# Performance work log

Hardware: AMD Instinct MI355X
Metric: run time of the kernel (lower is better)

The kernel has to match this reference:

```python
import jax, jax.numpy as jnp
import numpy as np

NUM_HEADS = 128
QK_NOPE = 128
QK_ROPE = 64
V_HEAD = 128
Q_HEAD_DIM = 192
SOFTMAX_SCALE = 1.0 / np.sqrt(192.0)


def _rope_interleave(x, cos, sin):
    # x: [b,h,s,d]; reorder interleaved pairs to half-split layout then rotate
    b, h, s, d = x.shape
    x = x.reshape(b, h, s, d // 2, 2).swapaxes(3, 4).reshape(b, h, s, d)
    x1, x2 = x[..., : d // 2], x[..., d // 2:]
    rot = jnp.concatenate([-x2, x1], axis=-1)
    return x * cos + rot * sin


def setup_inputs() -> dict:
    key = jax.random.key(0)
    ks = jax.random.split(key, 8)
    bsz, q_len = 16, 1
    q_lora, kv_lora = 1536, 512
    cache_cap = 4096
    start_pos = 2048
    s = 0.05
    q_normed_dn = jax.random.normal(ks[0], (bsz, q_len, q_lora), jnp.float32) * s
    compressed_kv = jax.random.normal(ks[1], (bsz, q_len, kv_lora), jnp.float32) * s
    k_pe = jax.random.normal(ks[2], (bsz, 1, q_len, QK_ROPE), jnp.float32) * s
    position_ids = jnp.full((bsz, q_len), start_pos, dtype=jnp.int64)
    ckv_cache = jax.random.normal(ks[3], (bsz, cache_cap, kv_lora), jnp.float32) * s
    k_pe_cache = jax.random.normal(ks[4], (bsz, cache_cap, QK_ROPE), jnp.float32) * s
    # rope caches over full positions
    pos = jnp.arange(cache_cap, dtype=jnp.float32)
    inv = 1.0 / (10000.0 ** (jnp.arange(0, QK_ROPE, 2, dtype=jnp.float32) / QK_ROPE))
    freqs = pos[:, None] * inv[None, :]
    emb = jnp.concatenate([freqs, freqs], axis=-1)
    sin_cache = jnp.sin(emb)
    cos_cache = jnp.cos(emb)
    wkv_b = jax.random.normal(ks[5], (NUM_HEADS, QK_NOPE + V_HEAD, kv_lora), jnp.float32) * s
    wq_b = jax.random.normal(ks[6], (NUM_HEADS * Q_HEAD_DIM, q_lora), jnp.float32) * s
    return {
        "q_normed_dn": q_normed_dn,
        "compressed_kv": compressed_kv,
        "k_pe": k_pe,
        "position_ids": position_ids,
        "start_pos": start_pos,
        "ckv_cache": ckv_cache,
        "k_pe_cache": k_pe_cache,
        "sin_cache": sin_cache,
        "cos_cache": cos_cache,
        "wkv_b": wkv_b,
        "wq_b": wq_b,
    }


def reference(q_normed_dn, compressed_kv, k_pe, position_ids, start_pos,
              ckv_cache, k_pe_cache, sin_cache, cos_cache, wkv_b, wq_b):
    bsz, q_len, q_lora = q_normed_dn.shape
    kv_lora = compressed_kv.shape[-1]

    # split absorbed query projection
    wq_b_t = wq_b.T.reshape(q_lora, NUM_HEADS, Q_HEAD_DIM)  # [l,h,192]
    q_nope = jnp.einsum('bsl,lhd->bhsd', q_normed_dn, wq_b_t[:, :, :QK_NOPE])
    q_pe = jnp.einsum('bsl,lhd->bhsd', q_normed_dn, wq_b_t[:, :, QK_NOPE:])

    # matrix absorption: q_nope projected into latent space via w_ukv
    w_ukv = wkv_b[:, :QK_NOPE]                         # [h,128,c]
    q_nope = jnp.einsum('bshd,hdc->bshc', q_nope.swapaxes(1, 2), w_ukv)  # [b,s,h,c]

    # RoPE on q_pe and k_pe using gathered cos/sin at position_ids
    cos = cos_cache[position_ids][:, None]   # [b,1,s,d]
    sin = sin_cache[position_ids][:, None]
    q_pe = _rope_interleave(q_pe, cos, sin)            # [b,h,s,64]
    k_pe = _rope_interleave(k_pe, cos, sin)            # [b,1,s,64]
    q_pe = q_pe.swapaxes(1, 2)                         # [b,s,h,64]
    k_pe = k_pe[:, 0]                                  # [b,s,64]

    # append new tokens to caches at start_pos (q_len new tokens)
    ckv_cache = jax.lax.dynamic_update_slice(ckv_cache, compressed_kv, (0, start_pos, 0))
    k_pe_cache = jax.lax.dynamic_update_slice(k_pe_cache, k_pe, (0, start_pos, 0))
    kv_len = start_pos + q_len
    ckv = ckv_cache[:, :kv_len]                        # [b,n,c]
    kpe = k_pe_cache[:, :kv_len]                       # [b,n,64]

    # MLA decode attention in latent space (q_len==1, causal trivially satisfied)
    # scores = q_nope . ckv + q_pe . kpe
    scores = (jnp.einsum('bshc,bnc->bhsn', q_nope, ckv) +
              jnp.einsum('bshd,bnd->bhsn', q_pe, kpe)) * SOFTMAX_SCALE
    probs = jax.nn.softmax(scores, axis=-1)
    o = jnp.einsum('bhsn,bnc->bshc', probs, ckv)       # [b,s,h,c]
    o = o.reshape(bsz * q_len, NUM_HEADS, kv_lora)

    # project latent output to v_head_dim via tail of wkv_b
    attn_output = jnp.einsum('bhc,hdc->bhd', o, wkv_b[:, -V_HEAD:])
    return attn_output
```

## Files before the change

### kernel.cpp

```cpp
#include <hip/hip_runtime.h>
#include <hip/hip_bf16.h>
#include <math.h>

typedef __attribute__((ext_vector_type(8))) short short8x;
typedef __attribute__((ext_vector_type(4))) float f32x4;
typedef __attribute__((ext_vector_type(4))) unsigned short u16x4;
typedef __attribute__((ext_vector_type(8))) unsigned short u16x8;

#define NSPLIT 16
#define NTILE 66
#define KVROWS (NTILE * 32)

__device__ __forceinline__ unsigned short f2bf(float x) {
  unsigned int u = __float_as_uint(x);
  u += 0x7fffu + ((u >> 16) & 1u);
  return (unsigned short)(u >> 16);
}
__device__ __forceinline__ float bf2f(unsigned short u) {
  return __uint_as_float(((unsigned int)u) << 16);
}
__device__ __forceinline__ u16x4 cvt4(float4 v) {
  u16x4 r;
  r[0] = f2bf(v.x); r[1] = f2bf(v.y); r[2] = f2bf(v.z); r[3] = f2bf(v.w);
  return r;
}
__device__ __forceinline__ void gload_lds16(const void* g, void* l) {
  __builtin_amdgcn_global_load_lds(
      (const __attribute__((address_space(1))) unsigned int*)g,
      (__attribute__((address_space(3))) unsigned int*)l, 16, 0, 0);
}

__global__ __launch_bounds__(256, 6) void kA(
    const float* __restrict__ ckvc, const float* __restrict__ kpec,
    const float* __restrict__ ckvn, const float* __restrict__ kpein,
    const float* __restrict__ cosc, const float* __restrict__ sinc,
    const int* __restrict__ sposp, int cap,
    unsigned short* __restrict__ kvbf,
    const float* __restrict__ wq, const float* __restrict__ x,
    float* __restrict__ qpart) {
  const int bx = blockIdx.x;
  const int tid = threadIdx.x;

  if (bx < 1536) {
    const int rowblock = bx >> 2, kq = bx & 3;
    const int lane = tid & 63, wid = tid >> 6;
    const int l15 = lane & 15, lg = lane >> 4;
    const int rowb = rowblock * 64 + wid * 16;
    const float* wrow = wq + (size_t)(rowb + l15) * 1536 + kq * 384 + lg * 8;
    const float* xrow = x + (size_t)l15 * 1536 + kq * 384 + lg * 8;

    f32x4 aHH = (f32x4){0.f, 0.f, 0.f, 0.f};
    f32x4 aHL = (f32x4){0.f, 0.f, 0.f, 0.f};
    f32x4 aLH = (f32x4){0.f, 0.f, 0.f, 0.f};
    f32x4 bHH = (f32x4){0.f, 0.f, 0.f, 0.f};
    f32x4 bHL = (f32x4){0.f, 0.f, 0.f, 0.f};
    f32x4 bLH = (f32x4){0.f, 0.f, 0.f, 0.f};

    float4 wA[2], wB[2], xA[2], xB[2];
#pragma unroll
    for (int i = 0; i < 2; ++i) {
      wA[i] = *(const float4*)(wrow + i * 32);
      wB[i] = *(const float4*)(wrow + i * 32 + 4);
      xA[i] = *(const float4*)(xrow + i * 32);
      xB[i] = *(const float4*)(xrow + i * 32 + 4);
    }

#pragma unroll
    for (int kc = 0; kc < 12; ++kc) {
      const int s = kc & 1;
      const float wf[8] = {wA[s].x, wA[s].y, wA[s].z, wA[s].w,
                           wB[s].x, wB[s].y, wB[s].z, wB[s].w};
      const float xf[8] = {xA[s].x, xA[s].y, xA[s].z, xA[s].w,
                           xB[s].x, xB[s].y, xB[s].z, xB[s].w};
      short8x ah, al, bh, bl;
#pragma unroll
      for (int e = 0; e < 8; ++e) {
        const unsigned int wu = __float_as_uint(wf[e]);
        const float whf = __uint_as_float(wu & 0xffff0000u);
        ah[e] = (short)(wu >> 16);
        al[e] = (short)(__float_as_uint(wf[e] - whf) >> 16);
        const unsigned int xu = __float_as_uint(xf[e]);
        const float xhf = __uint_as_float(xu & 0xffff0000u);
        bh[e] = (short)(xu >> 16);
        bl[e] = (short)(__float_as_uint(xf[e] - xhf) >> 16);
      }
      if (kc + 2 < 12) {
        wA[s] = *(const float4*)(wrow + (kc + 2) * 32);
        wB[s] = *(const float4*)(wrow + (kc + 2) * 32 + 4);
        xA[s] = *(const float4*)(xrow + (kc + 2) * 32);
        xB[s] = *(const float4*)(xrow + (kc + 2) * 32 + 4);
      }
      if (kc & 1) {
        bHH = __builtin_amdgcn_mfma_f32_16x16x32_bf16(ah, bh, bHH, 0, 0, 0);
        bHL = __builtin_amdgcn_mfma_f32_16x16x32_bf16(ah, bl, bHL, 0, 0, 0);
        bLH = __builtin_amdgcn_mfma_f32_16x16x32_bf16(al, bh, bLH, 0, 0, 0);
      } else {
        aHH = __builtin_amdgcn_mfma_f32_16x16x32_bf16(ah, bh, aHH, 0, 0, 0);
        aHL = __builtin_amdgcn_mfma_f32_16x16x32_bf16(ah, bl, aHL, 0, 0, 0);
        aLH = __builtin_amdgcn_mfma_f32_16x16x32_bf16(al, bh, aLH, 0, 0, 0);
      }
    }
    const f32x4 acc = (aHH + bHH) + (aHL + bHL) + (aLH + bLH);
#pragma unroll
    for (int r = 0; r < 4; ++r)
      qpart[(size_t)kq * 393216 + (size_t)l15 * 24576 + rowb + lg * 4 + r] = acc[r];
  } else {
    const int bxx = bx - 1536;
    const int spos = sposp[0];
#pragma unroll
    for (int i = 0; i < 8; ++i) {
      const int u = bxx * 2048 + i * 256 + tid;
      const int b = u / 304128;
      const int r = u - b * 304128;
      const int n = r / 144;
      const int c4 = (r - n * 144) * 4;
      float4 v = make_float4(0.f, 0.f, 0.f, 0.f);
      if (n < spos) {
        if (c4 < 512) v = *(const float4*)(ckvc + ((size_t)b * cap + n) * 512 + c4);
        else          v = *(const float4*)(kpec + ((size_t)b * cap + n) * 64 + (c4 - 512));
      } else if (n == spos) {
        if (c4 < 512) v = *(const float4*)(ckvn + (size_t)b * 512 + c4);
        else {
          const int d = c4 - 512;
          const float* kp = kpein + b * 64;
          float o[4];
          if (d < 32) {
#pragma unroll
            for (int k = 0; k < 4; ++k) {
              int j = d + k;
              o[k] = kp[2 * j] * cosc[spos * 64 + j] - kp[2 * j + 1] * sinc[spos * 64 + j];
            }
          } else {
#pragma unroll
            for (int k = 0; k < 4; ++k) {
              int j = d - 32 + k;
              o[k] = kp[2 * j + 1] * cosc[spos * 64 + j] + kp[2 * j] * sinc[spos * 64 + j];
            }
          }
          v = make_float4(o[0], o[1], o[2], o[3]);
        }
      }
      *(u16x4*)(kvbf + (size_t)u * 4) = cvt4(v);
    }
  }
}

__global__ __launch_bounds__(256) void kB2(
    const float* __restrict__ qpart, const float* __restrict__ wkv,
    const float* __restrict__ cosc, const float* __restrict__ sinc,
    const int* __restrict__ sposp, unsigned short* __restrict__ qcat,
    const unsigned short* __restrict__ kvbf, unsigned short* __restrict__ vT) {
  __shared__ __align__(16) unsigned char shbuf[36864];
  const int bx = blockIdx.x;
  const int tid = threadIdx.x;

  if (bx < 256) {
    float* qs = (float*)shbuf;
    const int h = bx & 127;
    const int half = bx >> 7;
    for (int u = tid; u < 2048; u += 256) {
      int bb = u >> 7, d = u & 127;
      const size_t off = (size_t)bb * 24576 + h * 192 + d;
      qs[u] = qpart[off] + qpart[off + 393216] +
              qpart[off + 786432] + qpart[off + 1179648];
    }
    __syncthreads();
    const int c = half * 256 + tid;
    float acc[16];
#pragma unroll
    for (int bb = 0; bb < 16; ++bb) acc[bb] = 0.f;
    const float* wbase = wkv + (size_t)h * 256 * 512;
    for (int d = 0; d < 128; ++d) {
      const float w = wbase[d * 512 + c];
#pragma unroll
      for (int bb = 0; bb < 16; ++bb) acc[bb] += qs[bb * 128 + d] * w;
    }
#pragma unroll
    for (int bb = 0; bb < 16; ++bb)
      qcat[(size_t)(bb * 128 + h) * 576 + c] = f2bf(acc[bb]);
  } else if (bx < 272) {
    const int b = bx - 256;
    const int pos = sposp[0];
#pragma unroll
    for (int i = 0; i < 16; ++i) {
      int idx = tid + i * 256;
      int h = idx >> 5, j = idx & 31;
      const float cj = cosc[pos * 64 + j];
      const float sj = sinc[pos * 64 + j];
      const size_t base = (size_t)b * 24576 + h * 192 + 128;
      float x0 = qpart[base + 2 * j] + qpart[base + 2 * j + 393216] +
                 qpart[base + 2 * j + 786432] + qpart[base + 2 * j + 1179648];
      float x1 = qpart[base + 2 * j + 1] + qpart[base + 2 * j + 1 + 393216] +
                 qpart[base + 2 * j + 1 + 786432] + qpart[base + 2 * j + 1 + 1179648];
      unsigned short* dst = qcat + (size_t)(b * 128 + h) * 576 + 512;
      dst[j] = f2bf(x0 * cj - x1 * sj);
      dst[j + 32] = f2bf(x1 * cj + x0 * sj);
    }
  } else {
    unsigned short* tile_sh = (unsigned short*)shbuf;
    const int v_ = bx - 272;
    const int b = v_ / NTILE;
    const int tile = v_ - b * NTILE;
    const int wid = tid >> 6;
    const unsigned short* src = kvbf + ((size_t)b * KVROWS + tile * 32) * 576;
#pragma unroll
    for (int i = 0; i < 9; ++i) {
      const int ch = i * 256 + tid;
      const int row = ch / 72, cc = ch - row * 72;
      gload_lds16(src + row * 576 + ((cc ^ (row & 7)) * 8),
                  &tile_sh[(i * 256 + wid * 64) * 8]);
    }
    __syncthreads();
    unsigned short* vdst = vT + ((size_t)b * NTILE + tile) * 18432;
#pragma unroll
    for (int r = 0; r < 9; ++r) {
      const int c = r * 64 + (tid >> 2);
      const int q = tid & 3;
      const int c8 = c >> 3, c7 = c & 7;
      u16x8 w;
#pragma unroll
      for (int j = 0; j < 8; ++j)
        w[j] = tile_sh[(q * 8 + j) * 576 + ((c8 ^ j) << 3) + c7];
      *(u16x8*)(vdst + c * 32 + q * 8) = w;
    }
  }
}

__global__ __launch_bounds__(512, 2) void k4_attn(
    const unsigned short* __restrict__ kvbf, const unsigned short* __restrict__ vT,
    const unsigned short* __restrict__ qcat, const int* __restrict__ sposp,
    unsigned short* __restrict__ opart, float* __restrict__ mlp) {
  __shared__ __align__(16) unsigned short kv_sh[2][32 * 576];
  __shared__ __align__(16) unsigned short vt_sh[2][512 * 32];
  __shared__ __align__(16) unsigned short p_sh[8 * 640];

  const int tid = threadIdx.x;
  const int split = blockIdx.x, b = blockIdx.y;
  const int kvlen = sposp[0] + 1;
  const int lane = tid & 63, wid = tid >> 6;
  const int l15 = lane & 15, lg = lane >> 4;

  const unsigned short* kvb = kvbf + (size_t)b * KVROWS * 576;
  const unsigned short* vtb = vT + (size_t)b * NTILE * 18432;

  const int vro = lane >> 2, vq = lane & 3;
  const int vgq = vq ^ ((vro >> 1) & 3);

  auto STAGE = [&](int pb, int tt) {
    const unsigned short* ksrc = kvb + (size_t)tt * 32 * 576;
    for (int j = wid; j < 36; j += 8) {
      int u = j * 64 + lane;
      int row = u / 72, cc = u - row * 72;
      gload_lds16(ksrc + row * 576 + ((cc ^ (row & 7)) * 8), &kv_sh[pb][j * 512]);
    }
    const unsigned short* vsrc = vtb + (size_t)tt * 18432;
    for (int j = wid; j < 32; j += 8)
      gload_lds16(vsrc + j * 512 + vro * 32 + vgq * 8, &vt_sh[pb][j * 512]);
  };

  STAGE(0, split);

  const int hrow = b * 128 + wid * 16 + l15;
  const unsigned short* qrow = qcat + (size_t)hrow * 576;
  short8x qf[18];
#pragma unroll
  for (int s = 0; s < 18; ++s)
    qf[s] = *(const short8x*)(qrow + s * 32 + lg * 8);

  f32x4 acc[32];
#pragma unroll
  for (int i = 0; i < 32; ++i) acc[i] = (f32x4){0.f, 0.f, 0.f, 0.f};
  float mold[4] = {-1e30f, -1e30f, -1e30f, -1e30f};
  float lsum[4] = {0.f, 0.f, 0.f, 0.f};
  const float C2 = (1.0f / sqrtf(192.0f)) * 1.4426950408889634f;

  const int vrd = ((lg ^ ((l15 >> 1) & 3)) << 3);

  int pb = 0;
  for (int tt = split; tt * 32 < kvlen; tt += NSPLIT, pb ^= 1) {
    __syncthreads();
    if ((tt + NSPLIT) * 32 < kvlen) STAGE(pb ^ 1, tt + NSPLIT);
    const int n0 = tt * 32;

    f32x4 D0 = (f32x4){0.f, 0.f, 0.f, 0.f};
    f32x4 D1 = (f32x4){0.f, 0.f, 0.f, 0.f};
#pragma unroll
    for (int s = 0; s < 18; ++s) {
      const int c8 = (s * 4 + lg) ^ (l15 & 7);
      short8x fb0 = *(const short8x*)&kv_sh[pb][l15 * 576 + c8 * 8];
      short8x fb1 = *(const short8x*)&kv_sh[pb][(16 + l15) * 576 + c8 * 8];
      D0 = __builtin_amdgcn_mfma_f32_16x16x32_bf16(qf[s], fb0, D0, 0, 0, 0);
      D1 = __builtin_amdgcn_mfma_f32_16x16x32_bf16(qf[s], fb1, D1, 0, 0, 0);
    }

    const bool v0 = (n0 + l15) < kvlen;
    const bool v1 = (n0 + 16 + l15) < kvlen;
    float alpha[4];
#pragma unroll
    for (int r = 0; r < 4; ++r) {
      const float t0 = v0 ? D0[r] * C2 : -1e30f;
      const float t1 = v1 ? D1[r] * C2 : -1e30f;
      float mx = fmaxf(t0, t1);
      mx = fmaxf(mx, __shfl_xor(mx, 1, 64));
      mx = fmaxf(mx, __shfl_xor(mx, 2, 64));
      mx = fmaxf(mx, __shfl_xor(mx, 4, 64));
      mx = fmaxf(mx, __shfl_xor(mx, 8, 64));
      const float mn = fmaxf(mold[r], mx);
      alpha[r] = exp2f(mold[r] - mn);
      const float p0 = v0 ? exp2f(t0 - mn) : 0.f;
      const float p1 = v1 ? exp2f(t1 - mn) : 0.f;
      float rs = p0 + p1;
      rs += __shfl_xor(rs, 1, 64);
      rs += __shfl_xor(rs, 2, 64);
      rs += __shfl_xor(rs, 4, 64);
      rs += __shfl_xor(rs, 8, 64);
      lsum[r] = lsum[r] * alpha[r] + rs;
      mold[r] = mn;
      p_sh[wid * 640 + (lg * 4 + r) * 40 + l15] = f2bf(p0);
      p_sh[wid * 640 + (lg * 4 + r) * 40 + 16 + l15] = f2bf(p1);
    }
    const f32x4 av = {alpha[0], alpha[1], alpha[2], alpha[3]};
#pragma unroll
    for (int cg = 0; cg < 32; ++cg) acc[cg] *= av;

    const short8x pa = *(const short8x*)&p_sh[wid * 640 + l15 * 40 + lg * 8];
#pragma unroll
    for (int cg = 0; cg < 32; ++cg) {
      short8x bv = *(const short8x*)&vt_sh[pb][cg * 512 + l15 * 32 + vrd];
      acc[cg] = __builtin_amdgcn_mfma_f32_16x16x32_bf16(pa, bv, acc[cg], 0, 0, 0);
    }
  }

  const int hbm_ = b * 128 + wid * 16 + lg * 4;
  if (l15 == 0) {
#pragma unroll
    for (int r = 0; r < 4; ++r) {
      mlp[(size_t)(hbm_ + r) * (2 * NSPLIT) + split * 2] = mold[r];
      mlp[(size_t)(hbm_ + r) * (2 * NSPLIT) + split * 2 + 1] = lsum[r];
    }
  }

  __syncthreads();
  unsigned short* ep = &kv_sh[0][0] + wid * 8192;
#pragma unroll
  for (int cg = 0; cg < 32; ++cg)
#pragma unroll
    for (int r = 0; r < 4; ++r)
      ep[(lg * 4 + r) * 512 + cg * 16 + l15] = f2bf(acc[cg][r]);
#pragma unroll
  for (int r16 = 0; r16 < 16; ++r16) {
    const int bh = b * 128 + wid * 16 + r16;
    const size_t ob = ((size_t)bh * NSPLIT + split) * 512;
#pragma unroll
    for (int i = 0; i < 2; ++i)
      *(u16x4*)&opart[ob + i * 256 + lane * 4] =
          *(const u16x4*)&ep[r16 * 512 + i * 256 + lane * 4];
  }
}

__global__ __launch_bounds__(512) void kC_out(
    const unsigned short* __restrict__ opart, const float* __restrict__ mlp,
    const float* __restrict__ wkv, float* __restrict__ out) {
  __shared__ float os[16 * 512];
  __shared__ float wsc[16 * 16];
  __shared__ float lsc[16];
  const int h = blockIdx.x;
  const int tid = threadIdx.x;

  if (tid < 16) {
    const int b = tid;
    const float* m = mlp + (size_t)(b * 128 + h) * (2 * NSPLIT);
    float mi[NSPLIT], li[NSPLIT], M = -1e30f;
#pragma unroll
    for (int i = 0; i < NSPLIT; ++i) {
      mi[i] = m[i * 2];
      li[i] = m[i * 2 + 1];
      M = fmaxf(M, mi[i]);
    }
    float Ls = 0.f;
#pragma unroll
    for (int i = 0; i < NSPLIT; ++i) {
      const float w = exp2f(mi[i] - M);
      Ls += li[i] * w;
      wsc[b * NSPLIT + i] = w;
    }
    lsc[b] = Ls;
  }
  __syncthreads();

  for (int u = tid; u < 8192; u += 512) {
    const int b = u >> 9, c = u & 511;
    const unsigned short* op = opart + (size_t)(b * 128 + h) * NSPLIT * 512 + c;
    float o = 0.f;
#pragma unroll
    for (int i = 0; i < NSPLIT; ++i) o += wsc[b * NSPLIT + i] * bf2f(op[i * 512]);
    os[u] = o / lsc[b];
  }
  __syncthreads();

  const int d = tid >> 2, cq = tid & 3;
  const float* wrow = wkv + ((size_t)(h * 256 + 128 + d)) * 512;
  float acc[16];
#pragma unroll
  for (int bb = 0; bb < 16; ++bb) acc[bb] = 0.f;
  for (int i = 0; i < 32; ++i) {
    const int c = cq * 4 + i * 16;
    const float4 w4 = *(const float4*)&wrow[c];
#pragma unroll
    for (int bb = 0; bb < 16; ++bb) {
      const float4 o4 = *(const float4*)&os[bb * 512 + c];
      acc[bb] += w4.x * o4.x + w4.y * o4.y + w4.z * o4.z + w4.w * o4.w;
    }
  }
#pragma unroll
  for (int bb = 0; bb < 16; ++bb) {
    float v = acc[bb];
    v += __shfl_xor(v, 1, 64);
    v += __shfl_xor(v, 2, 64);
    if (cq == 0) out[(size_t)(bb * 128 + h) * 128 + d] = v;
  }
}

extern "C" void kernel_launch(void* const* d_in, const int* in_sizes, int n_in,
                              void* d_out, int out_size, void* d_ws, size_t ws_size,
                              hipStream_t stream) {
  const float* x = (const float*)d_in[0];
  const float* ckvn = (const float*)d_in[1];
  const float* kpein = (const float*)d_in[2];
  const int* sposp = (const int*)d_in[4];
  const float* ckvc = (const float*)d_in[5];
  const float* kpec = (const float*)d_in[6];
  const float* sinc = (const float*)d_in[7];
  const float* cosc = (const float*)d_in[8];
  const float* wkv = (const float*)d_in[9];
  const float* wq = (const float*)d_in[10];
  float* out = (float*)d_out;

  const int cap = in_sizes[5] / (16 * 512);

  float* ws = (float*)d_ws;
  float* qpart = ws;
  float* mlp = ws + 1572864;
  unsigned short* qcat = (unsigned short*)(ws + 1638400);
  unsigned short* kvbf = (unsigned short*)(ws + 2228224);
  unsigned short* vT   = (unsigned short*)(ws + 11960320);
  unsigned short* opart = (unsigned short*)(ws + 21692416);

  kA<<<dim3(1536 + 2376), 256, 0, stream>>>(ckvc, kpec, ckvn, kpein, cosc, sinc,
                                            sposp, cap, kvbf, wq, x, qpart);
  kB2<<<dim3(272 + NTILE * 16), 256, 0, stream>>>(qpart, wkv, cosc, sinc, sposp,
                                                  qcat, kvbf, vT);
  k4_attn<<<dim3(NSPLIT, 16), 512, 0, stream>>>(kvbf, vT, qcat, sposp, opart, mlp);
  kC_out<<<dim3(128), 512, 0, stream>>>(opart, mlp, wkv, out);
}
```

Baseline: 171.0 us.

## Fuse KV transpose into attention kernel, dropping separate vT buffer pass

Removes the kB2 blocks that transposed each bf16 KV tile into a global vT buffer. The attention kernel now builds the transposed V tile in LDS from the already-staged KV tile, with an extra barrier before the PV MMA. This saves a global write and re-read of the transposed cache but adds in-loop LDS transpose work and a sync per tile. Launch bounds drop to one block per CU because of the larger LDS footprint.

```diff
diff --git a/kernel.cpp b/kernel.cpp
--- a/kernel.cpp
+++ b/kernel.cpp
@@ -148,14 +148,12 @@
 __global__ __launch_bounds__(256) void kB2(
     const float* __restrict__ qpart, const float* __restrict__ wkv,
     const float* __restrict__ cosc, const float* __restrict__ sinc,
-    const int* __restrict__ sposp, unsigned short* __restrict__ qcat,
-    const unsigned short* __restrict__ kvbf, unsigned short* __restrict__ vT) {
-  __shared__ __align__(16) unsigned char shbuf[36864];
+    const int* __restrict__ sposp, unsigned short* __restrict__ qcat) {
+  __shared__ float qs[16 * 128];
   const int bx = blockIdx.x;
   const int tid = threadIdx.x;
 
   if (bx < 256) {
-    float* qs = (float*)shbuf;
     const int h = bx & 127;
     const int half = bx >> 7;
     for (int u = tid; u < 2048; u += 256) {
@@ -178,7 +176,7 @@
 #pragma unroll
     for (int bb = 0; bb < 16; ++bb)
       qcat[(size_t)(bb * 128 + h) * 576 + c] = f2bf(acc[bb]);
-  } else if (bx < 272) {
+  } else {
     const int b = bx - 256;
     const int pos = sposp[0];
 #pragma unroll
@@ -196,43 +194,18 @@
       dst[j] = f2bf(x0 * cj - x1 * sj);
       dst[j + 32] = f2bf(x1 * cj + x0 * sj);
     }
-  } else {
-    unsigned short* tile_sh = (unsigned short*)shbuf;
-    const int v_ = bx - 272;
-    const int b = v_ / NTILE;
-    const int tile = v_ - b * NTILE;
-    const int wid = tid >> 6;
-    const unsigned short* src = kvbf + ((size_t)b * KVROWS + tile * 32) * 576;
-#pragma unroll
-    for (int i = 0; i < 9; ++i) {
-      const int ch = i * 256 + tid;
-      const int row = ch / 72, cc = ch - row * 72;
-      gload_lds16(src + row * 576 + ((cc ^ (row & 7)) * 8),
-                  &tile_sh[(i * 256 + wid * 64) * 8]);
-    }
-    __syncthreads();
-    unsigned short* vdst = vT + ((size_t)b * NTILE + tile) * 18432;
-#pragma unroll
-    for (int r = 0; r < 9; ++r) {
-      const int c = r * 64 + (tid >> 2);
-      const int q = tid & 3;
-      const int c8 = c >> 3, c7 = c & 7;
-      u16x8 w;
-#pragma unroll
-      for (int j = 0; j < 8; ++j)
-        w[j] = tile_sh[(q * 8 + j) * 576 + ((c8 ^ j) << 3) + c7];
-      *(u16x8*)(vdst + c * 32 + q * 8) = w;
-    }
-  }
-}
-
-__global__ __launch_bounds__(512, 2) void k4_attn(
-    const unsigned short* __restrict__ kvbf, const unsigned short* __restrict__ vT,
+  }
+}
+
+__global__ __launch_bounds__(512, 1) void k4_attn(
+    const unsigned short* __restrict__ kvbf,
     const unsigned short* __restrict__ qcat, const int* __restrict__ sposp,
     unsigned short* __restrict__ opart, float* __restrict__ mlp) {
-  __shared__ __align__(16) unsigned short kv_sh[2][32 * 576];
-  __shared__ __align__(16) unsigned short vt_sh[2][512 * 32];
-  __shared__ __align__(16) unsigned short p_sh[8 * 640];
+  __shared__ __align__(16) unsigned short lds_all[65536];
+  unsigned short* const kv0 = lds_all;
+  unsigned short* const kv1 = lds_all + 18432;
+  unsigned short* const vt_sh = lds_all + 36864;
+  unsigned short* const p_sh = lds_all + 53248;
 
   const int tid = threadIdx.x;
   const int split = blockIdx.x, b = blockIdx.y;
@@ -241,24 +214,17 @@
   const int l15 = lane & 15, lg = lane >> 4;
 
   const unsigned short* kvb = kvbf + (size_t)b * KVROWS * 576;
-  const unsigned short* vtb = vT + (size_t)b * NTILE * 18432;
-
-  const int vro = lane >> 2, vq = lane & 3;
-  const int vgq = vq ^ ((vro >> 1) & 3);
-
-  auto STAGE = [&](int pb, int tt) {
+
+  auto STAGE = [&](unsigned short* dst, int tt) {
     const unsigned short* ksrc = kvb + (size_t)tt * 32 * 576;
     for (int j = wid; j < 36; j += 8) {
       int u = j * 64 + lane;
       int row = u / 72, cc = u - row * 72;
-      gload_lds16(ksrc + row * 576 + ((cc ^ (row & 7)) * 8), &kv_sh[pb][j * 512]);
-    }
-    const unsigned short* vsrc = vtb + (size_t)tt * 18432;
-    for (int j = wid; j < 32; j += 8)
-      gload_lds16(vsrc + j * 512 + vro * 32 + vgq * 8, &vt_sh[pb][j * 512]);
+      gload_lds16(ksrc + row * 576 + ((cc ^ (row & 7)) * 8), dst + j * 512);
+    }
   };
 
-  STAGE(0, split);
+  STAGE(kv0, split);
 
   const int hrow = b * 128 + wid * 16 + l15;
   const unsigned short* qrow = qcat + (size_t)hrow * 576;
@@ -278,17 +244,32 @@
 
   int pb = 0;
   for (int tt = split; tt * 32 < kvlen; tt += NSPLIT, pb ^= 1) {
+    unsigned short* const kvcur = pb ? kv1 : kv0;
+    unsigned short* const kvnxt = pb ? kv0 : kv1;
     __syncthreads();
-    if ((tt + NSPLIT) * 32 < kvlen) STAGE(pb ^ 1, tt + NSPLIT);
+    if ((tt + NSPLIT) * 32 < kvlen) STAGE(kvnxt, tt + NSPLIT);
     const int n0 = tt * 32;
+
+#pragma unroll
+    for (int r5 = 0; r5 < 5; ++r5) {
+      const int idx = r5 * 512 + tid;
+      if (idx < 2304) {
+        const int c = idx >> 2, q = idx & 3;
+        u16x8 w;
+#pragma unroll
+        for (int j = 0; j < 8; ++j)
+          w[j] = kvcur[(q * 8 + j) * 576 + (((c >> 3) ^ j) << 3) + (c & 7)];
+        *(u16x8*)&vt_sh[c * 32 + ((q ^ ((c >> 1) & 3)) << 3)] = w;
+      }
+    }
 
     f32x4 D0 = (f32x4){0.f, 0.f, 0.f, 0.f};
     f32x4 D1 = (f32x4){0.f, 0.f, 0.f, 0.f};
 #pragma unroll
     for (int s = 0; s < 18; ++s) {
       const int c8 = (s * 4 + lg) ^ (l15 & 7);
-      short8x fb0 = *(const short8x*)&kv_sh[pb][l15 * 576 + c8 * 8];
-      short8x fb1 = *(const short8x*)&kv_sh[pb][(16 + l15) * 576 + c8 * 8];
+      short8x fb0 = *(const short8x*)&kvcur[l15 * 576 + c8 * 8];
+      short8x fb1 = *(const short8x*)&kvcur[(16 + l15) * 576 + c8 * 8];
       D0 = __builtin_amdgcn_mfma_f32_16x16x32_bf16(qf[s], fb0, D0, 0, 0, 0);
       D1 = __builtin_amdgcn_mfma_f32_16x16x32_bf16(qf[s], fb1, D1, 0, 0, 0);
     }
@@ -323,10 +304,12 @@
 #pragma unroll
     for (int cg = 0; cg < 32; ++cg) acc[cg] *= av;
 
+    __syncthreads();
+
     const short8x pa = *(const short8x*)&p_sh[wid * 640 + l15 * 40 + lg * 8];
 #pragma unroll
     for (int cg = 0; cg < 32; ++cg) {
-      short8x bv = *(const short8x*)&vt_sh[pb][cg * 512 + l15 * 32 + vrd];
+      short8x bv = *(const short8x*)&vt_sh[cg * 512 + l15 * 32 + vrd];
       acc[cg] = __builtin_amdgcn_mfma_f32_16x16x32_bf16(pa, bv, acc[cg], 0, 0, 0);
     }
   }
@@ -341,7 +324,7 @@
   }
 
   __syncthreads();
-  unsigned short* ep = &kv_sh[0][0] + wid * 8192;
+  unsigned short* ep = lds_all + wid * 8192;
 #pragma unroll
   for (int cg = 0; cg < 32; ++cg)
 #pragma unroll
@@ -443,13 +426,11 @@
   float* mlp = ws + 1572864;
   unsigned short* qcat = (unsigned short*)(ws + 1638400);
   unsigned short* kvbf = (unsigned short*)(ws + 2228224);
-  unsigned short* vT   = (unsigned short*)(ws + 11960320);
-  unsigned short* opart = (unsigned short*)(ws + 21692416);
+  unsigned short* opart = (unsigned short*)(ws + 11960320);
 
   kA<<<dim3(1536 + 2376), 256, 0, stream>>>(ckvc, kpec, ckvn, kpein, cosc, sinc,
                                             sposp, cap, kvbf, wq, x, qpart);
-  kB2<<<dim3(272 + NTILE * 16), 256, 0, stream>>>(qpart, wkv, cosc, sinc, sposp,
-                                                  qcat, kvbf, vT);
-  k4_attn<<<dim3(NSPLIT, 16), 512, 0, stream>>>(kvbf, vT, qcat, sposp, opart, mlp);
+  kB2<<<dim3(272), 256, 0, stream>>>(qpart, wkv, cosc, sinc, sposp, qcat);
+  k4_attn<<<dim3(NSPLIT, 16), 512, 0, stream>>>(kvbf, qcat, sposp, opart, mlp);
   kC_out<<<dim3(128), 512, 0, stream>>>(opart, mlp, wkv, out);
 }
```

New measurement: 176.6 us. +3.3%, slower.

## Drop KV double buffering in attention kernel to shrink LDS footprint

Applied to the files above, without the earlier changes.

Replaces the double-buffered K and V LDS staging with a single buffer that is loaded synchronously each iteration, bracketed by barriers. The output epilogue is split into two passes so it fits in the smaller shared allocation. This cuts LDS per block roughly in half so two 512-thread blocks could co-reside on a CU. In exchange, global-to-LDS loads no longer overlap with the MFMA work of the previous tile. With only 256 blocks in the grid, the extra occupancy may go unused.

```diff
diff --git a/kernel.cpp b/kernel.cpp
--- a/kernel.cpp
+++ b/kernel.cpp
@@ -230,9 +230,10 @@
     const unsigned short* __restrict__ kvbf, const unsigned short* __restrict__ vT,
     const unsigned short* __restrict__ qcat, const int* __restrict__ sposp,
     unsigned short* __restrict__ opart, float* __restrict__ mlp) {
-  __shared__ __align__(16) unsigned short kv_sh[2][32 * 576];
-  __shared__ __align__(16) unsigned short vt_sh[2][512 * 32];
-  __shared__ __align__(16) unsigned short p_sh[8 * 640];
+  __shared__ __align__(16) unsigned short lds_all[39936];
+  unsigned short* const kv_sh = lds_all;
+  unsigned short* const vt_sh = lds_all + 18432;
+  unsigned short* const p_sh = lds_all + 34816;
 
   const int tid = threadIdx.x;
   const int split = blockIdx.x, b = blockIdx.y;
@@ -246,19 +247,17 @@
   const int vro = lane >> 2, vq = lane & 3;
   const int vgq = vq ^ ((vro >> 1) & 3);
 
-  auto STAGE = [&](int pb, int tt) {
+  auto STAGE = [&](int tt) {
     const unsigned short* ksrc = kvb + (size_t)tt * 32 * 576;
     for (int j = wid; j < 36; j += 8) {
       int u = j * 64 + lane;
       int row = u / 72, cc = u - row * 72;
-      gload_lds16(ksrc + row * 576 + ((cc ^ (row & 7)) * 8), &kv_sh[pb][j * 512]);
+      gload_lds16(ksrc + row * 576 + ((cc ^ (row & 7)) * 8), kv_sh + j * 512);
     }
     const unsigned short* vsrc = vtb + (size_t)tt * 18432;
     for (int j = wid; j < 32; j += 8)
-      gload_lds16(vsrc + j * 512 + vro * 32 + vgq * 8, &vt_sh[pb][j * 512]);
+      gload_lds16(vsrc + j * 512 + vro * 32 + vgq * 8, vt_sh + j * 512);
   };
-
-  STAGE(0, split);
 
   const int hrow = b * 128 + wid * 16 + l15;
   const unsigned short* qrow = qcat + (size_t)hrow * 576;
@@ -276,10 +275,10 @@
 
   const int vrd = ((lg ^ ((l15 >> 1) & 3)) << 3);
 
-  int pb = 0;
-  for (int tt = split; tt * 32 < kvlen; tt += NSPLIT, pb ^= 1) {
-    __syncthreads();
-    if ((tt + NSPLIT) * 32 < kvlen) STAGE(pb ^ 1, tt + NSPLIT);
+  for (int tt = split; tt * 32 < kvlen; tt += NSPLIT) {
+    __syncthreads();
+    STAGE(tt);
+    __syncthreads();
     const int n0 = tt * 32;
 
     f32x4 D0 = (f32x4){0.f, 0.f, 0.f, 0.f};
@@ -287,8 +286,8 @@
 #pragma unroll
     for (int s = 0; s < 18; ++s) {
       const int c8 = (s * 4 + lg) ^ (l15 & 7);
-      short8x fb0 = *(const short8x*)&kv_sh[pb][l15 * 576 + c8 * 8];
-      short8x fb1 = *(const short8x*)&kv_sh[pb][(16 + l15) * 576 + c8 * 8];
+      short8x fb0 = *(const short8x*)&kv_sh[l15 * 576 + c8 * 8];
+      short8x fb1 = *(const short8x*)&kv_sh[(16 + l15) * 576 + c8 * 8];
       D0 = __builtin_amdgcn_mfma_f32_16x16x32_bf16(qf[s], fb0, D0, 0, 0, 0);
       D1 = __builtin_amdgcn_mfma_f32_16x16x32_bf16(qf[s], fb1, D1, 0, 0, 0);
     }
@@ -326,7 +325,7 @@
     const short8x pa = *(const short8x*)&p_sh[wid * 640 + l15 * 40 + lg * 8];
 #pragma unroll
     for (int cg = 0; cg < 32; ++cg) {
-      short8x bv = *(const short8x*)&vt_sh[pb][cg * 512 + l15 * 32 + vrd];
+      short8x bv = *(const short8x*)&vt_sh[cg * 512 + l15 * 32 + vrd];
       acc[cg] = __builtin_amdgcn_mfma_f32_16x16x32_bf16(pa, bv, acc[cg], 0, 0, 0);
     }
   }
@@ -340,21 +339,27 @@
     }
   }
 
-  __syncthreads();
-  unsigned short* ep = &kv_sh[0][0] + wid * 8192;
-#pragma unroll
-  for (int cg = 0; cg < 32; ++cg)
-#pragma unroll
-    for (int r = 0; r < 4; ++r)
-      ep[(lg * 4 + r) * 512 + cg * 16 + l15] = f2bf(acc[cg][r]);
-#pragma unroll
-  for (int r16 = 0; r16 < 16; ++r16) {
-    const int bh = b * 128 + wid * 16 + r16;
-    const size_t ob = ((size_t)bh * NSPLIT + split) * 512;
-#pragma unroll
-    for (int i = 0; i < 2; ++i)
-      *(u16x4*)&opart[ob + i * 256 + lane * 4] =
-          *(const u16x4*)&ep[r16 * 512 + i * 256 + lane * 4];
+#pragma unroll
+  for (int p2 = 0; p2 < 2; ++p2) {
+    __syncthreads();
+    unsigned short* ep = lds_all + wid * 4096;
+    if ((lg >> 1) == p2) {
+#pragma unroll
+      for (int cg = 0; cg < 32; ++cg)
+#pragma unroll
+        for (int r = 0; r < 4; ++r)
+          ep[(((lg & 1) * 4) + r) * 512 + cg * 16 + l15] = f2bf(acc[cg][r]);
+    }
+    __syncthreads();
+#pragma unroll
+    for (int r8 = 0; r8 < 8; ++r8) {
+      const int bh = b * 128 + wid * 16 + p2 * 8 + r8;
+      const size_t ob = ((size_t)bh * NSPLIT + split) * 512;
+#pragma unroll
+      for (int i = 0; i < 2; ++i)
+        *(u16x4*)&opart[ob + i * 256 + lane * 4] =
+            *(const u16x4*)&ep[r8 * 512 + i * 256 + lane * 4];
+    }
   }
 }
 
```

New measurement: 173.0 us. Within noise of the previous version (+1.2%).

## Fuse KV bf16 conversion and V transpose into kA via LDS tile staging

Applied to the files above, without the earlier changes.

The KV-cache conversion in kA now works per 32-row tile. Each tile is staged in fp32 through a 72KB LDS buffer, and the kernel writes both the row-major bf16 KV and the transposed V layout straight from that staging. The separate transpose pass in kB2, which re-read the bf16 KV from global memory, is removed, saving one global round trip of the KV data. In exchange, kA's LDS use is large, so its occupancy hint drops from 6 to 2 blocks, which may slow the co-scheduled q-projection GEMM blocks in the same launch.

```diff
diff --git a/kernel.cpp b/kernel.cpp
--- a/kernel.cpp
+++ b/kernel.cpp
@@ -30,14 +30,15 @@
       (__attribute__((address_space(3))) unsigned int*)l, 16, 0, 0);
 }
 
-__global__ __launch_bounds__(256, 6) void kA(
+__global__ __launch_bounds__(256, 2) void kA(
     const float* __restrict__ ckvc, const float* __restrict__ kpec,
     const float* __restrict__ ckvn, const float* __restrict__ kpein,
     const float* __restrict__ cosc, const float* __restrict__ sinc,
     const int* __restrict__ sposp, int cap,
-    unsigned short* __restrict__ kvbf,
+    unsigned short* __restrict__ kvbf, unsigned short* __restrict__ vT,
     const float* __restrict__ wq, const float* __restrict__ x,
     float* __restrict__ qpart) {
+  __shared__ __align__(16) float lf[18432];
   const int bx = blockIdx.x;
   const int tid = threadIdx.x;
 
@@ -106,41 +107,121 @@
       qpart[(size_t)kq * 393216 + (size_t)l15 * 24576 + rowb + lg * 4 + r] = acc[r];
   } else {
     const int bxx = bx - 1536;
+    const int b = bxx / NTILE;
+    const int tile = bxx - b * NTILE;
+    const int n0 = tile * 32;
     const int spos = sposp[0];
-#pragma unroll
-    for (int i = 0; i < 8; ++i) {
-      const int u = bxx * 2048 + i * 256 + tid;
-      const int b = u / 304128;
-      const int r = u - b * 304128;
-      const int n = r / 144;
-      const int c4 = (r - n * 144) * 4;
-      float4 v = make_float4(0.f, 0.f, 0.f, 0.f);
-      if (n < spos) {
-        if (c4 < 512) v = *(const float4*)(ckvc + ((size_t)b * cap + n) * 512 + c4);
-        else          v = *(const float4*)(kpec + ((size_t)b * cap + n) * 64 + (c4 - 512));
-      } else if (n == spos) {
-        if (c4 < 512) v = *(const float4*)(ckvn + (size_t)b * 512 + c4);
-        else {
-          const int d = c4 - 512;
-          const float* kp = kpein + b * 64;
-          float o[4];
-          if (d < 32) {
-#pragma unroll
-            for (int k = 0; k < 4; ++k) {
-              int j = d + k;
-              o[k] = kp[2 * j] * cosc[spos * 64 + j] - kp[2 * j + 1] * sinc[spos * 64 + j];
+    unsigned short* kdst = kvbf + ((size_t)b * KVROWS + n0) * 576;
+    unsigned short* vdst = vT + ((size_t)b * NTILE + tile) * 18432;
+
+    if (n0 + 31 < spos) {
+      const float* cbase = ckvc + ((size_t)b * cap + n0) * 512;
+      const float* pbase = kpec + ((size_t)b * cap + n0) * 64;
+#pragma unroll
+      for (int i = 0; i < 18; ++i) {
+        const int ch = i * 256 + tid;
+        const int row = ch / 144, cc = ch - row * 144;
+        const int gc = cc ^ (row & 7);
+        const float* s = (gc < 128) ? cbase + (size_t)row * 512 + gc * 4
+                                    : pbase + (size_t)row * 64 + (gc - 128) * 4;
+        gload_lds16(s, &lf[(i * 256 + (tid >> 6) * 64) * 4]);
+      }
+      __syncthreads();
+#pragma unroll
+      for (int g = 0; g < 9; ++g) {
+        const int u = g * 256 + tid;
+        const int row = u / 72, p = u - row * 72;
+        const float4 a  = *(const float4*)&lf[(row * 144 + ((2 * p) ^ (row & 7))) * 4];
+        const float4 c2 = *(const float4*)&lf[(row * 144 + ((2 * p + 1) ^ (row & 7))) * 4];
+        const u16x4 lo = cvt4(a), hi = cvt4(c2);
+        u16x8 w;
+#pragma unroll
+        for (int k = 0; k < 4; ++k) { w[k] = lo[k]; w[4 + k] = hi[k]; }
+        *(u16x8*)(kdst + (size_t)u * 8) = w;
+      }
+#pragma unroll
+      for (int r = 0; r < 9; ++r) {
+        const int c = r * 64 + (tid >> 2);
+        const int q = tid & 3;
+        const int gc = c >> 2, c3 = c & 3;
+        u16x8 w;
+#pragma unroll
+        for (int j = 0; j < 8; ++j) {
+          const int n = q * 8 + j;
+          w[j] = f2bf(lf[(n * 144 + (gc ^ j)) * 4 + c3]);
+        }
+        *(u16x8*)(vdst + c * 32 + q * 8) = w;
+      }
+    } else if (n0 <= spos) {
+#pragma unroll
+      for (int i = 0; i < 18; ++i) {
+        const int u = i * 256 + tid;
+        const int row = u / 144, c4 = (u - row * 144) * 4;
+        const int n = n0 + row;
+        float4 v = make_float4(0.f, 0.f, 0.f, 0.f);
+        if (n < spos) {
+          if (c4 < 512) v = *(const float4*)(ckvc + ((size_t)b * cap + n) * 512 + c4);
+          else          v = *(const float4*)(kpec + ((size_t)b * cap + n) * 64 + (c4 - 512));
+        } else if (n == spos) {
+          if (c4 < 512) v = *(const float4*)(ckvn + (size_t)b * 512 + c4);
+          else {
+            const int d = c4 - 512;
+            const float* kp = kpein + b * 64;
+            float o[4];
+            if (d < 32) {
+#pragma unroll
+              for (int k = 0; k < 4; ++k) {
+                int j = d + k;
+                o[k] = kp[2 * j] * cosc[spos * 64 + j] - kp[2 * j + 1] * sinc[spos * 64 + j];
+              }
+            } else {
+#pragma unroll
+              for (int k = 0; k < 4; ++k) {
+                int j = d - 32 + k;
+                o[k] = kp[2 * j + 1] * cosc[spos * 64 + j] + kp[2 * j] * sinc[spos * 64 + j];
+              }
             }
-          } else {
-#pragma unroll
-            for (int k = 0; k < 4; ++k) {
-              int j = d - 32 + k;
-              o[k] = kp[2 * j + 1] * cosc[spos * 64 + j] + kp[2 * j] * sinc[spos * 64 + j];
+            v = make_float4(o[0], o[1], o[2], o[3]);
+          }
+        }
+        *(u16x4*)(kdst + row * 576 + c4) = cvt4(v);
+      }
+#pragma unroll
+      for (int i = 0; i < 18; ++i) {
+        const int o = i * 256 + tid;
+        const int c = o >> 3;
+        const int n4 = (o & 7) * 4;
+        u16x4 w;
+#pragma unroll
+        for (int k = 0; k < 4; ++k) {
+          const int n = n0 + n4 + k;
+          float xv = 0.f;
+          if (n < spos) {
+            xv = (c < 512) ? ckvc[((size_t)b * cap + n) * 512 + c]
+                           : kpec[((size_t)b * cap + n) * 64 + (c - 512)];
+          } else if (n == spos) {
+            if (c < 512) xv = ckvn[(size_t)b * 512 + c];
+            else {
+              const int d = c - 512;
+              const float* kp = kpein + b * 64;
+              const int j = (d < 32) ? d : d - 32;
+              const float cj = cosc[spos * 64 + j], sj = sinc[spos * 64 + j];
+              xv = (d < 32) ? kp[2 * j] * cj - kp[2 * j + 1] * sj
+                            : kp[2 * j + 1] * cj + kp[2 * j] * sj;
             }
           }
-          v = make_float4(o[0], o[1], o[2], o[3]);
+          w[k] = f2bf(xv);
         }
-      }
-      *(u16x4*)(kvbf + (size_t)u * 4) = cvt4(v);
+        *(u16x4*)(vdst + c * 32 + n4) = w;
+      }
+    } else {
+      const u16x8 z = {0, 0, 0, 0, 0, 0, 0, 0};
+#pragma unroll
+      for (int i = 0; i < 9; ++i) {
+        const int oc = i * 256 + tid;
+        *(u16x8*)(kdst + oc * 8) = z;
+        *(u16x8*)(vdst + oc * 8) = z;
+      }
     }
   }
 }
@@ -148,14 +229,12 @@
 __global__ __launch_bounds__(256) void kB2(
     const float* __restrict__ qpart, const float* __restrict__ wkv,
     const float* __restrict__ cosc, const float* __restrict__ sinc,
-    const int* __restrict__ sposp, unsigned short* __restrict__ qcat,
-    const unsigned short* __restrict__ kvbf, unsigned short* __restrict__ vT) {
-  __shared__ __align__(16) unsigned char shbuf[36864];
+    const int* __restrict__ sposp, unsigned short* __restrict__ qcat) {
+  __shared__ float qs[16 * 128];
   const int bx = blockIdx.x;
   const int tid = threadIdx.x;
 
   if (bx < 256) {
-    float* qs = (float*)shbuf;
     const int h = bx & 127;
     const int half = bx >> 7;
     for (int u = tid; u < 2048; u += 256) {
@@ -178,7 +257,7 @@
 #pragma unroll
     for (int bb = 0; bb < 16; ++bb)
       qcat[(size_t)(bb * 128 + h) * 576 + c] = f2bf(acc[bb]);
-  } else if (bx < 272) {
+  } else {
     const int b = bx - 256;
     const int pos = sposp[0];
 #pragma unroll
@@ -195,33 +274,6 @@
       unsigned short* dst = qcat + (size_t)(b * 128 + h) * 576 + 512;
       dst[j] = f2bf(x0 * cj - x1 * sj);
       dst[j + 32] = f2bf(x1 * cj + x0 * sj);
-    }
-  } else {
-    unsigned short* tile_sh = (unsigned short*)shbuf;
-    const int v_ = bx - 272;
-    const int b = v_ / NTILE;
-    const int tile = v_ - b * NTILE;
-    const int wid = tid >> 6;
-    const unsigned short* src = kvbf + ((size_t)b * KVROWS + tile * 32) * 576;
-#pragma unroll
-    for (int i = 0; i < 9; ++i) {
-      const int ch = i * 256 + tid;
-      const int row = ch / 72, cc = ch - row * 72;
-      gload_lds16(src + row * 576 + ((cc ^ (row & 7)) * 8),
-                  &tile_sh[(i * 256 + wid * 64) * 8]);
-    }
-    __syncthreads();
-    unsigned short* vdst = vT + ((size_t)b * NTILE + tile) * 18432;
-#pragma unroll
-    for (int r = 0; r < 9; ++r) {
-      const int c = r * 64 + (tid >> 2);
-      const int q = tid & 3;
-      const int c8 = c >> 3, c7 = c & 7;
-      u16x8 w;
-#pragma unroll
-      for (int j = 0; j < 8; ++j)
-        w[j] = tile_sh[(q * 8 + j) * 576 + ((c8 ^ j) << 3) + c7];
-      *(u16x8*)(vdst + c * 32 + q * 8) = w;
     }
   }
 }
@@ -446,10 +498,10 @@
   unsigned short* vT   = (unsigned short*)(ws + 11960320);
   unsigned short* opart = (unsigned short*)(ws + 21692416);
 
-  kA<<<dim3(1536 + 2376), 256, 0, stream>>>(ckvc, kpec, ckvn, kpein, cosc, sinc,
-                                            sposp, cap, kvbf, wq, x, qpart);
-  kB2<<<dim3(272 + NTILE * 16), 256, 0, stream>>>(qpart, wkv, cosc, sinc, sposp,
-                                                  qcat, kvbf, vT);
+  kA<<<dim3(1536 + NTILE * 16), 256, 0, stream>>>(ckvc, kpec, ckvn, kpein,
+                                                  cosc, sinc, sposp, cap,
+                                                  kvbf, vT, wq, x, qpart);
+  kB2<<<dim3(272), 256, 0, stream>>>(qpart, wkv, cosc, sinc, sposp, qcat);
   k4_attn<<<dim3(NSPLIT, 16), 512, 0, stream>>>(kvbf, vT, qcat, sposp, opart, mlp);
   kC_out<<<dim3(128), 512, 0, stream>>>(opart, mlp, wkv, out);
 }
```

Measured after the change: 164.2 us. -4.0%, faster.
